# Performance work log

Hardware: AMD Instinct MI355X
Metric: run time of the kernel (lower is better)

## Reference

```python
import jax, jax.numpy as jnp
import numpy as np

H = 1024      # hidden_dim
NH = 16       # num_heads
HD = H // NH  # head_dim
FF = 4 * H
EPS = 1e-5

def _ln(x, g, b):
    m = jnp.mean(x, axis=-1, keepdims=True)
    v = jnp.var(x, axis=-1, keepdims=True)
    return (x - m) * jax.lax.rsqrt(v + EPS) * g + b

def setup_inputs() -> dict:
    key = jax.random.key(0)
    ks = jax.random.split(key, 12)
    s = 1.0 / np.sqrt(H)
    inp = {
        'x': jax.random.normal(ks[0], (2, 2048, H), dtype=jnp.float32),
        'Wq': jax.random.normal(ks[1], (H, H), dtype=jnp.float32) * s,
        'bq': jnp.zeros((H,), dtype=jnp.float32),
        'Wk': jax.random.normal(ks[2], (H, H), dtype=jnp.float32) * s,
        'bk': jnp.zeros((H,), dtype=jnp.float32),
        'Wv': jax.random.normal(ks[3], (H, H), dtype=jnp.float32) * s,
        'bv': jnp.zeros((H,), dtype=jnp.float32),
        'Wo': jax.random.normal(ks[4], (H, H), dtype=jnp.float32) * s,
        'bo': jnp.zeros((H,), dtype=jnp.float32),
        'g1': jnp.ones((H,), dtype=jnp.float32),
        'b1': jnp.zeros((H,), dtype=jnp.float32),
        'W1': jax.random.normal(ks[5], (H, FF), dtype=jnp.float32) * s,
        'bf1': jnp.zeros((FF,), dtype=jnp.float32),
        'W2': jax.random.normal(ks[6], (FF, H), dtype=jnp.float32) * (1.0 / np.sqrt(FF)),
        'bf2': jnp.zeros((H,), dtype=jnp.float32),
        'g2': jnp.ones((H,), dtype=jnp.float32),
        'b2': jnp.zeros((H,), dtype=jnp.float32),
    }
    return inp

def reference(x, Wq, bq, Wk, bk, Wv, bv, Wo, bo, g1, b1, W1, bf1, W2, bf2, g2, b2):
    B, S, _ = x.shape
    residual = x
    xn = _ln(x, g1, b1)
    # [B,S,H] -> [B,NH,S,HD]
    def split_heads(t):
        return t.reshape(B, S, NH, HD).transpose(0, 2, 1, 3)
    q = split_heads(xn @ Wq + bq)
    k = split_heads(xn @ Wk + bk)
    v = split_heads(xn @ Wv + bv)
    scores = jnp.einsum('bhqd,bhkd->bhqk', q, k) / np.sqrt(HD).astype(np.float32)
    attn = jax.nn.softmax(scores, axis=-1)
    ctx = jnp.einsum('bhqk,bhkd->bhqd', attn, v)
    ctx = ctx.transpose(0, 2, 1, 3).reshape(B, S, H)
    out = ctx @ Wo + bo + residual
    residual = out
    on = _ln(out, g2, b2)
    out = jax.nn.relu(on @ W1 + bf1) @ W2 + bf2 + residual
    return out
```

## Files before the change

kernel.cpp:

```cpp
#include <hip/hip_runtime.h>
#include <hip/hip_bf16.h>

constexpr int HDIM = 1024;
constexpr int NHEAD = 16;
constexpr int FFDIM = 4096;
constexpr int SEQLEN = 2048;
constexpr int NTOK = 4096;

typedef __bf16 bf16x8 __attribute__((ext_vector_type(8)));
typedef float f32x4 __attribute__((ext_vector_type(4)));
typedef short s16x4 __attribute__((ext_vector_type(4)));

union U16x8 {
    s16x4 h[2];
    bf16x8 v;
    int4 raw;
    unsigned u[4];
    short s[8];
};

__device__ __forceinline__ short f2bf(float f) {
    union { float f; unsigned u; } c;
    c.f = f;
    return (short)((c.u + 0x8000u) >> 16);
}
__device__ __forceinline__ float bf2f(short s) {
    union { unsigned u; float f; } c;
    c.u = ((unsigned)(unsigned short)s) << 16;
    return c.f;
}

__device__ __forceinline__ unsigned cvtpk(float a, float b) {
    __hip_bfloat162 h = __float22bfloat162_rn(float2{a, b});
    return *reinterpret_cast<unsigned*>(&h);
}

__device__ __forceinline__ float exp2_raw(float x) {
    float r;
    asm("v_exp_f32 %0, %1" : "=v"(r) : "v"(x));
    return r;
}

template <int N>
__device__ __forceinline__ void wait_vmcnt() {
    if constexpr (N == 0) asm volatile("s_waitcnt vmcnt(0)" ::: "memory");
    else if constexpr (N == 8) asm volatile("s_waitcnt vmcnt(8)" ::: "memory");
    else if constexpr (N == 16) asm volatile("s_waitcnt vmcnt(16)" ::: "memory");
    else static_assert(N == 0 || N == 8 || N == 16, "unsupported vmcnt");
}
__device__ __forceinline__ void barrier_fence() {
    __builtin_amdgcn_s_barrier();
    asm volatile("" ::: "memory");
}

__device__ __forceinline__ void gload16(const void* gsrc, void* lds) {
    __builtin_amdgcn_global_load_lds(
        (const __attribute__((address_space(1))) unsigned int*)gsrc,
        (__attribute__((address_space(3))) unsigned int*)lds, 16, 0, 0);
}


constexpr float QSCALE = 0.18033688011112042f;

__device__ __forceinline__ void ln_store(float (&vv)[16], const float* g,
                                         const float* b, short* orow, int lane,
                                         float mean, float rstd) {
#pragma unroll
    for (int i = 0; i < 4; ++i) {
        const int c = i * 256 + lane * 4;
        float4 gv = *(const float4*)&g[c];
        float4 bv = *(const float4*)&b[c];
        union { s16x4 h4; uint2 u2; } pk;
        pk.u2.x = cvtpk((vv[i * 4 + 0] - mean) * rstd * gv.x + bv.x,
                        (vv[i * 4 + 1] - mean) * rstd * gv.y + bv.y);
        pk.u2.y = cvtpk((vv[i * 4 + 2] - mean) * rstd * gv.z + bv.z,
                        (vv[i * 4 + 3] - mean) * rstd * gv.w + bv.w);
        const int kk = c & 31;
        const int dst = (c & ~31) + ((kk & 15) >> 2) * 8 + (kk >> 4) * 4;
        *(s16x4*)&orow[dst] = pk.h4;
    }
}

__device__ __forceinline__ void ln_row(const float* __restrict__ xr,
                                       const float* __restrict__ g,
                                       const float* __restrict__ b,
                                       short* __restrict__ orow, int lane) {
    float vv[16];
    float s = 0.0f, ss = 0.0f;
#pragma unroll
    for (int i = 0; i < 4; ++i) {
        float4 v = *(const float4*)&xr[i * 256 + lane * 4];
        vv[i * 4] = v.x; vv[i * 4 + 1] = v.y; vv[i * 4 + 2] = v.z; vv[i * 4 + 3] = v.w;
        s += v.x + v.y + v.z + v.w;
        ss += v.x * v.x + v.y * v.y + v.z * v.z + v.w * v.w;
    }
#pragma unroll
    for (int o = 32; o > 0; o >>= 1) {
        s += __shfl_xor(s, o);
        ss += __shfl_xor(ss, o);
    }
    const float mean = s * (1.0f / HDIM);
    const float rstd = rsqrtf(ss * (1.0f / HDIM) - mean * mean + 1e-5f);
    ln_store(vv, g, b, orow, lane, mean, rstd);
}

__device__ __forceinline__ void ln_row_b(const short* __restrict__ xr,
                                         const float* __restrict__ g,
                                         const float* __restrict__ b,
                                         short* __restrict__ orow, int lane) {
    float vv[16];
    float s = 0.0f, ss = 0.0f;
#pragma unroll
    for (int i = 0; i < 4; ++i) {
        s16x4 h = *(const s16x4*)&xr[i * 256 + lane * 4];
#pragma unroll
        for (int j = 0; j < 4; ++j) {
            const float f = bf2f(h[j]);
            vv[i * 4 + j] = f;
            s += f;
            ss += f * f;
        }
    }
#pragma unroll
    for (int o = 32; o > 0; o >>= 1) {
        s += __shfl_xor(s, o);
        ss += __shfl_xor(ss, o);
    }
    const float mean = s * (1.0f / HDIM);
    const float rstd = rsqrtf(ss * (1.0f / HDIM) - mean * mean + 1e-5f);
    ln_store(vv, g, b, orow, lane, mean, rstd);
}

__global__ __launch_bounds__(256)
void wconv_all(const float* __restrict__ Wq, const float* __restrict__ Wk,
               const float* __restrict__ Wv, const float* __restrict__ Wo,
               const float* __restrict__ W1, const float* __restrict__ W2,
               short* __restrict__ qkvT, short* __restrict__ WoT,
               short* __restrict__ W1T, short* __restrict__ W2T,
               const float* __restrict__ x, const float* __restrict__ g1,
               const float* __restrict__ b1, short* __restrict__ xn) {
    int i = blockIdx.x;
    if (i >= 6144) {
        const int wave = threadIdx.x >> 6, lane = threadIdx.x & 63;
        const int row = (i - 6144) * 4 + wave;
        ln_row(x + (size_t)row * HDIM, g1, b1, xn + (size_t)row * HDIM, lane);
        return;
    }
    const float* W;
    short* WT;
    int K, N, bx, by;
    if (i < 2048) {
        const int w = i >> 9;
        i &= 511;
        K = HDIM; N = HDIM; bx = i & 3; by = i >> 2;
        W = w == 0 ? Wq : w == 1 ? Wk : w == 2 ? Wv : Wo;
        WT = w == 3 ? WoT : qkvT + (size_t)w * HDIM * HDIM;
    } else if (i < 4096) {
        i -= 2048;
        K = HDIM; N = FFDIM; bx = i & 15; by = i >> 4;
        W = W1; WT = W1T;
    } else {
        i -= 4096;
        K = FFDIM; N = HDIM; bx = i & 3; by = i >> 2;
        W = W2; WT = W2T;
    }
    const int n = bx * 256 + threadIdx.x;
    const int g = by >> 2, fc = by & 3;
    const int k0 = g * 32 + fc * 4;
    float a[4], c[4];
#pragma unroll
    for (int j = 0; j < 4; ++j) a[j] = W[(size_t)(k0 + j) * N + n];
#pragma unroll
    for (int j = 0; j < 4; ++j) c[j] = W[(size_t)(k0 + 16 + j) * N + n];
    U16x8 u;
    u.u[0] = cvtpk(a[0], a[1]);
    u.u[1] = cvtpk(a[2], a[3]);
    u.u[2] = cvtpk(c[0], c[1]);
    u.u[3] = cvtpk(c[2], c[3]);
    *(int4*)(WT + (size_t)n * K + by * 8) = u.raw;
}

__global__ __launch_bounds__(256)
void ln_bf16b(const short* __restrict__ x, const float* __restrict__ g,
              const float* __restrict__ b, short* __restrict__ out) {
    const int wave = threadIdx.x >> 6, lane = threadIdx.x & 63;
    const int row = blockIdx.x * 4 + wave;
    ln_row_b(x + (size_t)row * HDIM, g, b, out + (size_t)row * HDIM, lane);
}

template <int BM, int BN, int MODE, int PIPE>
__global__ __launch_bounds__(256, (PIPE == 3) ? 1 : 2)
void gemm_bf16(const short* __restrict__ A, const short* __restrict__ BT,
               const float* __restrict__ bias, const void* __restrict__ resid,
               void* __restrict__ outp, int M, int N, int K,
               const float* __restrict__ bias2, const float* __restrict__ bias3,
               void* __restrict__ out3) {
    constexpr int MI = BM / 32, NJ = BN / 32;
    constexpr int NSEG = (BM + BN) / 16;
    constexpr int PW = NSEG / 4;
    constexpr int BUFS = (BM + BN) * 32;
    constexpr int NBUF = (PIPE == 3) ? 8 : 4;
    __shared__ short LdsF[NBUF * BUFS];
    const int tid = threadIdx.x;
    const int lane = tid & 63, wave = tid >> 6;
    const int wm = wave >> 1, wn = wave & 1;
    const int l15 = lane & 15, lg = lane >> 4;
    const int lsw = lg ^ ((l15 >> 1) & 3);
    const int m0 = blockIdx.x * BM, n0 = blockIdx.y * BN;
    const int nk = K >> 5;
    const int sr = lane >> 2;
    const int sc8 = (((lane & 3) ^ ((sr >> 1) & 3))) * 8;

    auto stage = [&](int buf, int kt) {
#pragma unroll
        for (int p = 0; p < PW; ++p) {
            const int s = wave + p * 4;
            const short* src = (s < BM / 16)
                ? A + (size_t)(m0 + s * 16 + sr) * K + kt * 32 + sc8
                : BT + (size_t)(n0 + (s - BM / 16) * 16 + sr) * K + kt * 32 + sc8;
            const int off = __builtin_amdgcn_readfirstlane(buf * BUFS * 2 + s * 1024);
            gload16(src, (char*)LdsF + off);
        }
    };
    auto compute = [&](int buf, f32x4 (&acc)[MI][NJ]) {
        bf16x8 af[MI], bfr[NJ];
#pragma unroll
        for (int i = 0; i < MI; ++i)
            af[i] = *(const bf16x8*)&LdsF[buf * BUFS +
                                          (wm * (BM / 2) + i * 16 + l15) * 32 + lsw * 8];
#pragma unroll
        for (int j = 0; j < NJ; ++j)
            bfr[j] = *(const bf16x8*)&LdsF[buf * BUFS +
                                           (BM + wn * (BN / 2) + j * 16 + l15) * 32 + lsw * 8];
#pragma unroll
        for (int i = 0; i < MI; ++i)
#pragma unroll
            for (int j = 0; j < NJ; ++j)
                acc[i][j] = __builtin_amdgcn_mfma_f32_16x16x32_bf16(af[i], bfr[j], acc[i][j], 0, 0, 0);
    };

    f32x4 acc[MI][NJ] = {};
    if constexpr (PIPE == 2) {
        stage(0, 0); stage(1, 1); stage(2, 2); stage(3, 3);
        const int np = nk >> 1;
        for (int t = 0; t < np; ++t) {
            const int pb = (t & 1) * 2;
            if (t + 1 < np) wait_vmcnt<8>();
            else wait_vmcnt<0>();
            barrier_fence();
            __builtin_amdgcn_s_setprio(1);
            compute(pb, acc);
            compute(pb + 1, acc);
            __builtin_amdgcn_s_setprio(0);
            if (t + 2 < np) {
                barrier_fence();
                stage(pb, 2 * t + 4);
                stage(pb + 1, 2 * t + 5);
            }
        }
    } else {
        stage(0, 0); stage(1, 1); stage(2, 2); stage(3, 3);
        stage(4, 4); stage(5, 5);
        const int np = nk >> 1;
        for (int t = 0; t < np; ++t) {
            const int pb = (t & 3) * 2;
            if (t + 2 < np) wait_vmcnt<16>();
            else if (t + 1 < np) wait_vmcnt<8>();
            else wait_vmcnt<0>();
            barrier_fence();
            if (t + 3 < np) {
                const int sb = ((t + 3) & 3) * 2;
                stage(sb, 2 * t + 6);
                stage(sb + 1, 2 * t + 7);
            }
            __builtin_amdgcn_s_setprio(1);
            compute(pb, acc);
            compute(pb + 1, acc);
            __builtin_amdgcn_s_setprio(0);
        }
    }

    const int rbase = m0 + wm * (BM / 2);
    const int cbase = n0 + wn * (BN / 2);
    if constexpr (MODE == 4) {
#pragma unroll
        for (int i = 0; i < MI; ++i)
#pragma unroll
            for (int j = 0; j < NJ; ++j) {
                const int c = cbase + j * 16 + l15;
                const float bv = bias[c];
#pragma unroll
                for (int ii = 0; ii < 4; ++ii) {
                    const int r = rbase + i * 16 + lg * 4 + ii;
                    const size_t idx = (size_t)r * N + c;
                    ((short*)outp)[idx] = f2bf(acc[i][j][ii] + bv + ((const float*)resid)[idx]);
                }
            }
    } else if constexpr (MODE == 5) {
#pragma unroll
        for (int i = 0; i < MI; ++i)
#pragma unroll
            for (int j = 0; j < NJ; ++j) {
                const int c = cbase + j * 16 + l15;
                const float bv = bias[c];
#pragma unroll
                for (int ii = 0; ii < 4; ++ii) {
                    const int r = rbase + i * 16 + lg * 4 + ii;
                    const size_t idx = (size_t)r * N + c;
                    ((float*)outp)[idx] = acc[i][j][ii] + bv + bf2f(((const short*)resid)[idx]);
                }
            }
    } else if constexpr (MODE == 1) {
#pragma unroll
        for (int i = 0; i < MI; ++i)
#pragma unroll
            for (int j = 0; j < NJ; ++j) {
                const int c = cbase + j * 16 + l15;
                const float bv = bias[c];
                const int cp = (c & ~31) | ((l15 >> 2) * 8 + (j & 1) * 4 + (l15 & 3));
#pragma unroll
                for (int ii = 0; ii < 4; ++ii) {
                    const int r = rbase + i * 16 + lg * 4 + ii;
                    float v = acc[i][j][ii] + bv;
                    v = v > 0.0f ? v : 0.0f;
                    ((short*)outp)[(size_t)r * N + cp] = f2bf(v);
                }
            }
    } else {
        const int which = n0 >> 10;
        if (which < 2) {
            const float* bb = which == 0 ? bias : bias2;
            const float qs = which == 0 ? QSCALE : 1.0f;
            short* QKp = (short*)outp;
#pragma unroll
            for (int i = 0; i < MI; ++i)
#pragma unroll
                for (int j = 0; j < NJ; ++j) {
                    const int c = cbase + j * 16 + l15;
                    const float bv = bb[c & 1023];
                    const int cp = (c & ~31) | ((l15 >> 2) * 8 + (j & 1) * 4 + (l15 & 3));
#pragma unroll
                    for (int ii = 0; ii < 4; ++ii) {
                        const int r = rbase + i * 16 + lg * 4 + ii;
                        QKp[(size_t)r * 2048 + cp] = f2bf((acc[i][j][ii] + bv) * qs);
                    }
                }
        } else {
            short* VTp = (short*)out3;
#pragma unroll
            for (int j = 0; j < NJ; ++j) {
                const int c = cbase + j * 16 + l15;
                const int cc = c - 2048;
                const int hh = cc >> 6, dd = cc & 63;
                const float bv = bias3[cc];
#pragma unroll
                for (int i = 0; i < MI; ++i) {
                    const int r0 = rbase + i * 16 + lg * 4;
                    const int bb_ = r0 >> 11;
                    const int s0 = r0 & (SEQLEN - 1);
                    const int sbase = (s0 & ~31) + lg * 8 + (i & 1) * 4;
                    union { s16x4 h4; uint2 u2; } pk;
                    pk.u2.x = cvtpk(acc[i][j][0] + bv, acc[i][j][1] + bv);
                    pk.u2.y = cvtpk(acc[i][j][2] + bv, acc[i][j][3] + bv);
                    *(s16x4*)&VTp[(((size_t)(bb_ * NHEAD + hh)) * 64 + dd) * SEQLEN + sbase] = pk.h4;
                }
            }
        }
    }
}

__global__ __launch_bounds__(512, 1)
void gemm256(const short* __restrict__ A, const short* __restrict__ BT,
             const float* __restrict__ bias, short* __restrict__ outp,
             int M, int N, int K) {
    constexpr int BM = 256, BN = 256;
    constexpr int MI = 8, NJ = 4;
    constexpr int PW = 4;
    constexpr int BUFS = (BM + BN) * 32;
    __shared__ short LdsF[4 * BUFS];
    const int tid = threadIdx.x;
    const int lane = tid & 63, wave = tid >> 6;
    const int wr = wave >> 2, wc = wave & 3;
    const int l15 = lane & 15, lg = lane >> 4;
    const int lsw = lg ^ ((l15 >> 1) & 3);
    const int m0 = blockIdx.x * BM, n0 = blockIdx.y * BN;
    const int nk = K >> 5;
    const int sr = lane >> 2;
    const int sc8 = (((lane & 3) ^ ((sr >> 1) & 3))) * 8;

    auto stage = [&](int buf, int kt) {
#pragma unroll
        for (int p = 0; p < PW; ++p) {
            const int s = wave + p * 8;
            const short* src = (s < 16)
                ? A + (size_t)(m0 + s * 16 + sr) * K + kt * 32 + sc8
                : BT + (size_t)(n0 + (s - 16) * 16 + sr) * K + kt * 32 + sc8;
            const int off = __builtin_amdgcn_readfirstlane(buf * BUFS * 2 + s * 1024);
            gload16(src, (char*)LdsF + off);
        }
    };
    auto compute = [&](int buf, f32x4 (&acc)[MI][NJ]) {
        bf16x8 af[MI], bfr[NJ];
#pragma unroll
        for (int i = 0; i < MI; ++i)
            af[i] = *(const bf16x8*)&LdsF[buf * BUFS +
                                          (wr * 128 + i * 16 + l15) * 32 + lsw * 8];
#pragma unroll
        for (int j = 0; j < NJ; ++j)
            bfr[j] = *(const bf16x8*)&LdsF[buf * BUFS +
                                           (BM + wc * 64 + j * 16 + l15) * 32 + lsw * 8];
#pragma unroll
        for (int i = 0; i < MI; ++i)
#pragma unroll
            for (int j = 0; j < NJ; ++j)
                acc[i][j] = __builtin_amdgcn_mfma_f32_16x16x32_bf16(af[i], bfr[j], acc[i][j], 0, 0, 0);
    };

    f32x4 acc[MI][NJ] = {};
    stage(0, 0); stage(1, 1); stage(2, 2); stage(3, 3);
    const int np = nk >> 1;
    for (int t = 0; t < np; ++t) {
        const int pb = (t & 1) * 2;
        if (t + 1 < np) wait_vmcnt<8>();
        else wait_vmcnt<0>();
        barrier_fence();
        __builtin_amdgcn_s_setprio(1);
        compute(pb, acc);
        compute(pb + 1, acc);
        __builtin_amdgcn_s_setprio(0);
        if (t + 2 < np) {
            barrier_fence();
            stage(pb, 2 * t + 4);
            stage(pb + 1, 2 * t + 5);
        }
    }

    const int rbase = m0 + wr * 128;
    const int cbase = n0 + wc * 64;
#pragma unroll
    for (int i = 0; i < MI; ++i)
#pragma unroll
        for (int j = 0; j < NJ; ++j) {
            const int c = cbase + j * 16 + l15;
            const float bv = bias[c];
            const int cp = (c & ~31) | ((l15 >> 2) * 8 + (j & 1) * 4 + (l15 & 3));
#pragma unroll
            for (int ii = 0; ii < 4; ++ii) {
                const int r = rbase + i * 16 + lg * 4 + ii;
                float v = acc[i][j][ii] + bv;
                v = v > 0.0f ? v : 0.0f;
                outp[(size_t)r * N + cp] = f2bf(v);
            }
        }
}

__global__ __launch_bounds__(256, 4)
void attn_fwd(const short* __restrict__ QK, const short* __restrict__ VT,
              short* __restrict__ ctx) {
    __shared__ short KlF[2 * 4096];
    __shared__ short VlF[2 * 4096];
    const int tid = threadIdx.x, lane = tid & 63, wave = tid >> 6;
    const int l15 = lane & 15, lg = lane >> 4;
    const int lsw = lg ^ ((l15 >> 1) & 3);
    const int bid = blockIdx.x;
    const int xcd = bid & 7, li = bid >> 3;
    const int bh = xcd * 4 + (li >> 5);
    const int qt = li & 31;
    const int b = bh >> 4, h = bh & 15;
    const size_t tokbase = (size_t)b * SEQLEN;
    const int sr = lane >> 2;
    const int sc8 = (((lane & 3) ^ ((sr >> 1) & 3))) * 8;

    const short* kp = QK + (tokbase + wave * 16 + sr) * 2048 + 1024 + h * 64 + sc8;
    const short* vp = VT + ((size_t)bh * 64 + wave * 16 + sr) * SEQLEN + sc8;

    auto stage = [&](int buf) {
        const int off = __builtin_amdgcn_readfirstlane(buf * 8192 + wave * 1024);
        gload16(kp, (char*)KlF + off);
        gload16(kp + 32, (char*)KlF + off + 4096);
        gload16(vp, (char*)VlF + off);
        gload16(vp + 32, (char*)VlF + off + 4096);
    };

    const short* qp = QK + (tokbase + qt * 64 + wave * 16 + l15) * 2048 + h * 64;
    bf16x8 qf[2];
    qf[0] = *(const bf16x8*)(qp + lg * 8);
    qf[1] = *(const bf16x8*)(qp + 32 + lg * 8);

    U16x8 uo;
#pragma unroll
    for (int j = 0; j < 8; ++j) uo.s[j] = 0x3F80;
    const bf16x8 onesv = uo.v;

    f32x4 o[4] = {};
    f32x4 Lacc = {};
    stage(0);
    for (int kt = 0; kt < SEQLEN / 64; ++kt) {
        const int buf = kt & 1;
        __syncthreads();
        if (kt + 1 < SEQLEN / 64) {
            kp += 64 * 2048;
            vp += 64;
            stage(buf ^ 1);
        }

        f32x4 sc[4];
        __builtin_amdgcn_s_setprio(1);
#pragma unroll
        for (int j = 0; j < 4; ++j) {
            bf16x8 kf0 = *(const bf16x8*)&KlF[buf * 4096 + (j * 16 + l15) * 32 + lsw * 8];
            bf16x8 kf1 = *(const bf16x8*)&KlF[buf * 4096 + 2048 + (j * 16 + l15) * 32 + lsw * 8];
            f32x4 z = {};
            z = __builtin_amdgcn_mfma_f32_16x16x32_bf16(kf0, qf[0], z, 0, 0, 0);
            sc[j] = __builtin_amdgcn_mfma_f32_16x16x32_bf16(kf1, qf[1], z, 0, 0, 0);
        }
        __builtin_amdgcn_s_setprio(0);

        U16x8 u0, u1;
        u0.u[0] = cvtpk(exp2_raw(sc[0][0]), exp2_raw(sc[0][1]));
        u0.u[1] = cvtpk(exp2_raw(sc[0][2]), exp2_raw(sc[0][3]));
        u0.u[2] = cvtpk(exp2_raw(sc[1][0]), exp2_raw(sc[1][1]));
        u0.u[3] = cvtpk(exp2_raw(sc[1][2]), exp2_raw(sc[1][3]));
        u1.u[0] = cvtpk(exp2_raw(sc[2][0]), exp2_raw(sc[2][1]));
        u1.u[1] = cvtpk(exp2_raw(sc[2][2]), exp2_raw(sc[2][3]));
        u1.u[2] = cvtpk(exp2_raw(sc[3][0]), exp2_raw(sc[3][1]));
        u1.u[3] = cvtpk(exp2_raw(sc[3][2]), exp2_raw(sc[3][3]));

        __builtin_amdgcn_s_setprio(1);
#pragma unroll
        for (int ks = 0; ks < 2; ++ks) {
            const bf16x8 pf = ks == 0 ? u0.v : u1.v;
            Lacc = __builtin_amdgcn_mfma_f32_16x16x32_bf16(onesv, pf, Lacc, 0, 0, 0);
#pragma unroll
            for (int fd = 0; fd < 4; ++fd) {
                bf16x8 vf = *(const bf16x8*)&VlF[buf * 4096 + ks * 2048 + (fd * 16 + l15) * 32 + lsw * 8];
                o[fd] = __builtin_amdgcn_mfma_f32_16x16x32_bf16(vf, pf, o[fd], 0, 0, 0);
            }
        }
        __builtin_amdgcn_s_setprio(0);
    }

    const float rl = 1.0f / Lacc[0];
    const int qrow = qt * 64 + wave * 16 + l15;
    short* crow = ctx + (tokbase + qrow) * HDIM + h * 64;
#pragma unroll
    for (int fd = 0; fd < 4; ++fd) {
        s16x4 v4;
#pragma unroll
        for (int ii = 0; ii < 4; ++ii) v4[ii] = f2bf(o[fd][ii] * rl);
        *(s16x4*)(crow + (fd >> 1) * 32 + lg * 8 + (fd & 1) * 4) = v4;
    }
}

extern "C" void kernel_launch(void* const* d_in, const int* in_sizes, int n_in,
                              void* d_out, int out_size, void* d_ws, size_t ws_size,
                              hipStream_t stream) {
    const float* x  = (const float*)d_in[0];
    const float* Wq = (const float*)d_in[1];
    const float* bq = (const float*)d_in[2];
    const float* Wk = (const float*)d_in[3];
    const float* bk = (const float*)d_in[4];
    const float* Wv = (const float*)d_in[5];
    const float* bv = (const float*)d_in[6];
    const float* Wo = (const float*)d_in[7];
    const float* bo = (const float*)d_in[8];
    const float* g1 = (const float*)d_in[9];
    const float* b1 = (const float*)d_in[10];
    const float* W1 = (const float*)d_in[11];
    const float* bf1 = (const float*)d_in[12];
    const float* W2 = (const float*)d_in[13];
    const float* bf2 = (const float*)d_in[14];
    const float* g2 = (const float*)d_in[15];
    const float* b2 = (const float*)d_in[16];

    char* ws = (char*)d_ws;
    const size_t MB = 1024 * 1024;
    short* qkvT = (short*)(ws + 0 * MB);
    short* WoT  = (short*)(ws + 6 * MB);
    short* W1T  = (short*)(ws + 8 * MB);
    short* W2T  = (short*)(ws + 16 * MB);
    short* xn   = (short*)(ws + 24 * MB);
    short* QKb  = (short*)(ws + 32 * MB);
    short* VTb  = (short*)(ws + 48 * MB);
    short* ctx  = (short*)(ws + 56 * MB);
    short* out1b = (short*)(ws + 64 * MB);
    short* h1   = (short*)(ws + 32 * MB);

    wconv_all<<<7168, 256, 0, stream>>>(Wq, Wk, Wv, Wo, W1, W2, qkvT, WoT, W1T,
                                        W2T, x, g1, b1, xn);

    gemm_bf16<128, 128, 2, 2><<<dim3(NTOK / 128, 3072 / 128), 256, 0, stream>>>(
        xn, qkvT, bq, nullptr, QKb, NTOK, 3072, HDIM, bk, bv, VTb);

    attn_fwd<<<1024, 256, 0, stream>>>(QKb, VTb, ctx);

    gemm_bf16<128, 128, 4, 3><<<dim3(NTOK / 128, HDIM / 128), 256, 0, stream>>>(
        ctx, WoT, bo, x, out1b, NTOK, HDIM, HDIM, nullptr, nullptr, nullptr);

    ln_bf16b<<<NTOK / 4, 256, 0, stream>>>(out1b, g2, b2, xn);

    gemm256<<<dim3(NTOK / 256, FFDIM / 256), 512, 0, stream>>>(
        xn, W1T, bf1, h1, NTOK, FFDIM, HDIM);

    gemm_bf16<128, 128, 5, 3><<<dim3(NTOK / 128, HDIM / 128), 256, 0, stream>>>(
        h1, W2T, bf2, out1b, (float*)d_out, NTOK, HDIM, FFDIM, nullptr, nullptr, nullptr);
}
```

Measured before the change: 211.9 us.

## Process two query tiles per attention block to reuse staged K/V fragments

Each attention block now handles 128 query rows (two 64-row sub-tiles) instead of 64, so every K/V tile staged into LDS and loaded into registers serves twice as many MFMA operations. This halves the grid to 512 blocks and relaxes launch bounds to 2 waves per SIMD to make room for the extra registers (two sets of accumulators and preloaded K/V fragments). It cuts global and LDS traffic per query, at the cost of lower occupancy and fewer blocks to spread across CUs.

```diff
diff --git a/kernel.cpp b/kernel.cpp
--- a/kernel.cpp
+++ b/kernel.cpp
@@ -454,7 +454,7 @@
         }
 }
 
-__global__ __launch_bounds__(256, 4)
+__global__ __launch_bounds__(256, 2)
 void attn_fwd(const short* __restrict__ QK, const short* __restrict__ VT,
               short* __restrict__ ctx) {
     __shared__ short KlF[2 * 4096];
@@ -464,8 +464,8 @@
     const int lsw = lg ^ ((l15 >> 1) & 3);
     const int bid = blockIdx.x;
     const int xcd = bid & 7, li = bid >> 3;
-    const int bh = xcd * 4 + (li >> 5);
-    const int qt = li & 31;
+    const int bh = xcd * 4 + (li >> 4);
+    const int qt = li & 15;
     const int b = bh >> 4, h = bh & 15;
     const size_t tokbase = (size_t)b * SEQLEN;
     const int sr = lane >> 2;
@@ -482,18 +482,21 @@
         gload16(vp + 32, (char*)VlF + off + 4096);
     };
 
-    const short* qp = QK + (tokbase + qt * 64 + wave * 16 + l15) * 2048 + h * 64;
-    bf16x8 qf[2];
-    qf[0] = *(const bf16x8*)(qp + lg * 8);
-    qf[1] = *(const bf16x8*)(qp + 32 + lg * 8);
+    bf16x8 qf[2][2];
+#pragma unroll
+    for (int qs = 0; qs < 2; ++qs) {
+        const short* qp = QK + (tokbase + qt * 128 + qs * 64 + wave * 16 + l15) * 2048 + h * 64;
+        qf[qs][0] = *(const bf16x8*)(qp + lg * 8);
+        qf[qs][1] = *(const bf16x8*)(qp + 32 + lg * 8);
+    }
 
     U16x8 uo;
 #pragma unroll
     for (int j = 0; j < 8; ++j) uo.s[j] = 0x3F80;
     const bf16x8 onesv = uo.v;
 
-    f32x4 o[4] = {};
-    f32x4 Lacc = {};
+    f32x4 o[2][4] = {};
+    f32x4 Lacc[2] = {};
     stage(0);
     for (int kt = 0; kt < SEQLEN / 64; ++kt) {
         const int buf = kt & 1;
@@ -504,51 +507,65 @@
             stage(buf ^ 1);
         }
 
-        f32x4 sc[4];
-        __builtin_amdgcn_s_setprio(1);
+        bf16x8 kf[4][2], vf[2][4];
 #pragma unroll
         for (int j = 0; j < 4; ++j) {
-            bf16x8 kf0 = *(const bf16x8*)&KlF[buf * 4096 + (j * 16 + l15) * 32 + lsw * 8];
-            bf16x8 kf1 = *(const bf16x8*)&KlF[buf * 4096 + 2048 + (j * 16 + l15) * 32 + lsw * 8];
-            f32x4 z = {};
-            z = __builtin_amdgcn_mfma_f32_16x16x32_bf16(kf0, qf[0], z, 0, 0, 0);
-            sc[j] = __builtin_amdgcn_mfma_f32_16x16x32_bf16(kf1, qf[1], z, 0, 0, 0);
-        }
-        __builtin_amdgcn_s_setprio(0);
-
-        U16x8 u0, u1;
-        u0.u[0] = cvtpk(exp2_raw(sc[0][0]), exp2_raw(sc[0][1]));
-        u0.u[1] = cvtpk(exp2_raw(sc[0][2]), exp2_raw(sc[0][3]));
-        u0.u[2] = cvtpk(exp2_raw(sc[1][0]), exp2_raw(sc[1][1]));
-        u0.u[3] = cvtpk(exp2_raw(sc[1][2]), exp2_raw(sc[1][3]));
-        u1.u[0] = cvtpk(exp2_raw(sc[2][0]), exp2_raw(sc[2][1]));
-        u1.u[1] = cvtpk(exp2_raw(sc[2][2]), exp2_raw(sc[2][3]));
-        u1.u[2] = cvtpk(exp2_raw(sc[3][0]), exp2_raw(sc[3][1]));
-        u1.u[3] = cvtpk(exp2_raw(sc[3][2]), exp2_raw(sc[3][3]));
-
-        __builtin_amdgcn_s_setprio(1);
-#pragma unroll
-        for (int ks = 0; ks < 2; ++ks) {
-            const bf16x8 pf = ks == 0 ? u0.v : u1.v;
-            Lacc = __builtin_amdgcn_mfma_f32_16x16x32_bf16(onesv, pf, Lacc, 0, 0, 0);
-#pragma unroll
-            for (int fd = 0; fd < 4; ++fd) {
-                bf16x8 vf = *(const bf16x8*)&VlF[buf * 4096 + ks * 2048 + (fd * 16 + l15) * 32 + lsw * 8];
-                o[fd] = __builtin_amdgcn_mfma_f32_16x16x32_bf16(vf, pf, o[fd], 0, 0, 0);
-            }
-        }
-        __builtin_amdgcn_s_setprio(0);
-    }
-
-    const float rl = 1.0f / Lacc[0];
-    const int qrow = qt * 64 + wave * 16 + l15;
-    short* crow = ctx + (tokbase + qrow) * HDIM + h * 64;
-#pragma unroll
-    for (int fd = 0; fd < 4; ++fd) {
-        s16x4 v4;
-#pragma unroll
-        for (int ii = 0; ii < 4; ++ii) v4[ii] = f2bf(o[fd][ii] * rl);
-        *(s16x4*)(crow + (fd >> 1) * 32 + lg * 8 + (fd & 1) * 4) = v4;
+            kf[j][0] = *(const bf16x8*)&KlF[buf * 4096 + (j * 16 + l15) * 32 + lsw * 8];
+            kf[j][1] = *(const bf16x8*)&KlF[buf * 4096 + 2048 + (j * 16 + l15) * 32 + lsw * 8];
+        }
+#pragma unroll
+        for (int ks = 0; ks < 2; ++ks)
+#pragma unroll
+            for (int fd = 0; fd < 4; ++fd)
+                vf[ks][fd] = *(const bf16x8*)&VlF[buf * 4096 + ks * 2048 + (fd * 16 + l15) * 32 + lsw * 8];
+
+#pragma unroll
+        for (int qs = 0; qs < 2; ++qs) {
+            f32x4 sc[4];
+            __builtin_amdgcn_s_setprio(1);
+#pragma unroll
+            for (int j = 0; j < 4; ++j) {
+                f32x4 z = {};
+                z = __builtin_amdgcn_mfma_f32_16x16x32_bf16(kf[j][0], qf[qs][0], z, 0, 0, 0);
+                sc[j] = __builtin_amdgcn_mfma_f32_16x16x32_bf16(kf[j][1], qf[qs][1], z, 0, 0, 0);
+            }
+            __builtin_amdgcn_s_setprio(0);
+
+            U16x8 u0, u1;
+            u0.u[0] = cvtpk(exp2_raw(sc[0][0]), exp2_raw(sc[0][1]));
+            u0.u[1] = cvtpk(exp2_raw(sc[0][2]), exp2_raw(sc[0][3]));
+            u0.u[2] = cvtpk(exp2_raw(sc[1][0]), exp2_raw(sc[1][1]));
+            u0.u[3] = cvtpk(exp2_raw(sc[1][2]), exp2_raw(sc[1][3]));
+            u1.u[0] = cvtpk(exp2_raw(sc[2][0]), exp2_raw(sc[2][1]));
+            u1.u[1] = cvtpk(exp2_raw(sc[2][2]), exp2_raw(sc[2][3]));
+            u1.u[2] = cvtpk(exp2_raw(sc[3][0]), exp2_raw(sc[3][1]));
+            u1.u[3] = cvtpk(exp2_raw(sc[3][2]), exp2_raw(sc[3][3]));
+
+            __builtin_amdgcn_s_setprio(1);
+#pragma unroll
+            for (int ks = 0; ks < 2; ++ks) {
+                const bf16x8 pf = ks == 0 ? u0.v : u1.v;
+                Lacc[qs] = __builtin_amdgcn_mfma_f32_16x16x32_bf16(onesv, pf, Lacc[qs], 0, 0, 0);
+#pragma unroll
+                for (int fd = 0; fd < 4; ++fd)
+                    o[qs][fd] = __builtin_amdgcn_mfma_f32_16x16x32_bf16(vf[ks][fd], pf, o[qs][fd], 0, 0, 0);
+            }
+            __builtin_amdgcn_s_setprio(0);
+        }
+    }
+
+#pragma unroll
+    for (int qs = 0; qs < 2; ++qs) {
+        const float rl = 1.0f / Lacc[qs][0];
+        const int qrow = qt * 128 + qs * 64 + wave * 16 + l15;
+        short* crow = ctx + (tokbase + qrow) * HDIM + h * 64;
+#pragma unroll
+        for (int fd = 0; fd < 4; ++fd) {
+            s16x4 v4;
+#pragma unroll
+            for (int ii = 0; ii < 4; ++ii) v4[ii] = f2bf(o[qs][fd][ii] * rl);
+            *(s16x4*)(crow + (fd >> 1) * 32 + lg * 8 + (fd & 1) * 4) = v4;
+        }
     }
 }
 
@@ -592,7 +609,7 @@
     gemm_bf16<128, 128, 2, 2><<<dim3(NTOK / 128, 3072 / 128), 256, 0, stream>>>(
         xn, qkvT, bq, nullptr, QKb, NTOK, 3072, HDIM, bk, bv, VTb);
 
-    attn_fwd<<<1024, 256, 0, stream>>>(QKb, VTb, ctx);
+    attn_fwd<<<512, 256, 0, stream>>>(QKb, VTb, ctx);
 
     gemm_bf16<128, 128, 4, 3><<<dim3(NTOK / 128, HDIM / 128), 256, 0, stream>>>(
         ctx, WoT, bo, x, out1b, NTOK, HDIM, HDIM, nullptr, nullptr, nullptr);
```

New measurement: 203.6 us (median of 3 runs). -3.9%, faster.
